# Kernel tuning notes

Hardware: AMD Instinct MI355X
Metric: run time of the kernel (lower is better)

The kernel has to match this reference:

```python
import jax, jax.numpy as jnp
import numpy as np
import math

# Dims: d_model=192, expand=2 -> d_inner=d_ssm=384, headdim=64 -> nheads=6,
# d_state=128, K=4 scan directions, ngroups=1 (directions fused into state dim).
D_MODEL = 192
D_STATE = 128
D_CONV = 3
EXPAND = 2
HEADDIM = 64
CHUNK = 256
D_INNER = EXPAND * D_MODEL          # 384
D_SSM = D_INNER                     # default d_ssm (d_mlp == 0)
NHEADS = D_SSM // HEADDIM           # 6
K = 4                               # scan directions
HTOT = K * NHEADS                   # 24 heads in the fused scan
NSTATE = K * D_STATE                # 512 fused state dim (ngroups=1)
CONV_BC = 2 * D_STATE + NHEADS      # 262
B, H, W = 2, 64, 64


def _dwconv(x, w, b):
    # x: (B,C,H,W), w: (C,1,k,k) depthwise, SAME padding ((k-1)//2)
    y = jax.lax.conv_general_dilated(
        x, w, (1, 1), [(1, 1), (1, 1)],
        feature_group_count=x.shape[1],
        dimension_numbers=('NCHW', 'OIHW', 'NCHW'))
    return y + b[None, :, None, None]


def _ssd(x, dt_raw, A_logs, Bm, Cm, Ds, dt_bias):
    # Mamba2 chunked selective scan (dt_softplus=True, default dt_limit).
    # x: (b,l,h,p)  dt_raw: (b,l,h)  Bm,Cm: (b,l,n) with ngroups=1
    A = -jnp.exp(A_logs)                              # (h,)
    dt = jax.nn.softplus(dt_raw + dt_bias)            # (b,l,h)
    b, l, h, p = x.shape
    n = Bm.shape[-1]
    nc = l // CHUNK
    xc = x.reshape(b, nc, CHUNK, h, p)
    dtc = dt.reshape(b, nc, CHUNK, h)
    Bc = Bm.reshape(b, nc, CHUNK, n)
    Cc = Cm.reshape(b, nc, CHUNK, n)
    dA = dtc * A                                      # (b,nc,cs,h)
    acum = jnp.cumsum(dA, axis=2)
    # intra-chunk (causal, attention-like)
    a_t = jnp.transpose(acum, (0, 1, 3, 2))           # (b,nc,h,cs)
    diff = a_t[..., :, None] - a_t[..., None, :]      # (b,nc,h,i,j)
    causal = jnp.tril(jnp.ones((CHUNK, CHUNK), bool))
    Lmat = jnp.where(causal, jnp.exp(diff), 0.0)
    CB = jnp.einsum('bcin,bcjn->bcij', Cc, Bc)        # (b,nc,i,j)
    M = CB[:, :, None] * Lmat * jnp.transpose(dtc, (0, 1, 3, 2))[:, :, :, None, :]
    y = jnp.einsum('bchij,bcjhp->bcihp', M, xc)
    # chunk-final states
    decay_end = jnp.exp(acum[:, :, -1:, :] - acum)    # (b,nc,cs,h)
    states = jnp.einsum('bcjh,bcjn,bcjhp->bchpn', decay_end * dtc, Bc, xc)
    chunk_decay = jnp.exp(acum[:, :, -1, :])          # (b,nc,h)

    def step(S, inp):
        st, dec = inp
        return S * dec[:, :, None, None] + st, S

    S0 = jnp.zeros((b, h, p, n), x.dtype)
    _, prev = jax.lax.scan(step, S0, (jnp.moveaxis(states, 1, 0),
                                      jnp.moveaxis(chunk_decay, 1, 0)))
    prev = jnp.moveaxis(prev, 0, 1)                   # (b,nc,h,p,n)
    y = y + jnp.einsum('bcih,bcin,bchpn->bcihp', jnp.exp(acum), Cc, prev)
    y = y + xc * Ds[:, None]                          # D skip connection
    return y.reshape(b, l, h, p)


def _branch(u, u_cross, W_skip, W_xs, W_bcdt, conv_xs_w, conv_xs_b,
            conv_bc_w, conv_bc_b, dt_bias, A_logs, Ds, norm_w, W_out):
    Bb, Hh, Ww, _ = u.shape
    L = Hh * Ww
    z = (u @ W_skip).reshape(Bb, L, D_SSM)            # gate (d_mlp == 0)
    xs = jnp.transpose(u @ W_xs, (0, 3, 1, 2))        # (B,d_ssm,H,W)
    xs = jax.nn.silu(_dwconv(xs, conv_xs_w, conv_xs_b))
    bc = jnp.transpose(u_cross @ W_bcdt, (0, 3, 1, 2))
    bc = jax.nn.silu(_dwconv(bc, conv_bc_w, conv_bc_b))
    xbc = jnp.concatenate([xs, bc], axis=1)           # (B,646,H,W)
    C = xbc.shape[1]
    v = xbc.reshape(Bb, C, L)                         # HW raster
    vt = jnp.transpose(xbc, (0, 1, 3, 2)).reshape(Bb, C, L)  # WH raster
    hw = jnp.stack([v, vt], axis=1)                   # (B,2,C,L)
    xbcdt = jnp.concatenate([hw, jnp.flip(hw, axis=-1)], axis=1)  # (B,4,C,L)
    xp = xbcdt[:, :, :D_SSM]
    Bp = xbcdt[:, :, D_SSM:D_SSM + D_STATE]
    Cp = xbcdt[:, :, D_SSM + D_STATE:D_SSM + 2 * D_STATE]
    dtp = xbcdt[:, :, D_SSM + 2 * D_STATE:]
    x = xp.reshape(Bb, K * D_SSM, L).transpose(0, 2, 1).reshape(Bb, L, HTOT, HEADDIM)
    Bm = Bp.reshape(Bb, NSTATE, L).transpose(0, 2, 1)
    Cm = Cp.reshape(Bb, NSTATE, L).transpose(0, 2, 1)
    dt = dtp.reshape(Bb, HTOT, L).transpose(0, 2, 1)
    y = _ssd(x, dt, A_logs, Bm, Cm, Ds, dt_bias)      # (B,L,24,64)
    y = y.reshape(Bb, L, K, D_SSM)
    out_y = y[:, :, 0]
    inv_y = jnp.flip(y[:, :, 2:4], axis=1)            # (B,L,2,d_ssm)
    wh_y = y[:, :, 1].reshape(Bb, Ww, Hh, D_SSM).transpose(0, 2, 1, 3).reshape(Bb, L, D_SSM)
    invwh_y = inv_y[:, :, 1].reshape(Bb, Ww, Hh, D_SSM).transpose(0, 2, 1, 3).reshape(Bb, L, D_SSM)
    yf = out_y + inv_y[:, :, 0] + wh_y + invwh_y
    # gated RMSNorm (norm_before_gate=False, group_size == d_ssm)
    g = yf * jax.nn.silu(z)
    g = g * jax.lax.rsqrt(jnp.mean(g * g, axis=-1, keepdims=True) + 1e-5) * norm_w
    return (g @ W_out).reshape(Bb, Hh, Ww, D_MODEL)


def setup_inputs():
    key = jax.random.key(0)
    ks = jax.random.split(key, 16)
    f = lambda i, s: jax.random.normal(ks[i], s, jnp.float32)
    sc = 0.02
    dt = jnp.exp(jax.random.uniform(ks[10], (NHEADS,)) *
                 (math.log(0.1) - math.log(0.001)) + math.log(0.001))
    dt = jnp.maximum(dt, 1e-4)
    inv_dt = dt + jnp.log(-jnp.expm1(-dt))
    A = jax.random.uniform(ks[11], (NHEADS,), minval=1.0, maxval=16.0)
    return {
        'u1': f(0, (B, H, W, D_MODEL)),
        'u2': f(1, (B, H, W, D_MODEL)),
        'u2_cat_u1': f(2, (B, H, W, D_MODEL)),
        'u1_cat_u2': f(3, (B, H, W, D_MODEL)),
        'W_skip': f(4, (D_MODEL, D_SSM)) * sc,
        'W_xs': f(5, (D_MODEL, D_SSM)) * sc,
        'W_bcdt': f(6, (D_MODEL, CONV_BC)) * sc,
        'conv_xs_w': f(7, (D_SSM, 1, D_CONV, D_CONV)) * sc,
        'conv_xs_b': jnp.zeros((D_SSM,), jnp.float32),
        'conv_bc_w': f(8, (CONV_BC, 1, D_CONV, D_CONV)) * sc,
        'conv_bc_b': jnp.zeros((CONV_BC,), jnp.float32),
        'dt_bias': jnp.tile(inv_dt, K),
        'A_logs': jnp.tile(jnp.log(A), K),
        'Ds': jnp.ones((HTOT,), jnp.float32),
        'norm_w': jnp.ones((D_SSM,), jnp.float32),
        'W_out': f(9, (D_SSM, D_MODEL)) * sc,
    }


def reference(u1, u2, u2_cat_u1, u1_cat_u2, W_skip, W_xs, W_bcdt,
              conv_xs_w, conv_xs_b, conv_bc_w, conv_bc_b,
              dt_bias, A_logs, Ds, norm_w, W_out):
    args = (W_skip, W_xs, W_bcdt, conv_xs_w, conv_xs_b, conv_bc_w,
            conv_bc_b, dt_bias, A_logs, Ds, norm_w, W_out)
    out1 = _branch(u1, u2_cat_u1, *args)
    out2 = _branch(u2, u1_cat_u2, *args)
    return out1, out2
```

## Files before the change

### kernel.cpp

```cpp
#include <hip/hip_runtime.h>
#include <hip/hip_bf16.h>

#define DEV __device__ __forceinline__

static constexpr int LL   = 4096;
static constexpr int GG   = 4;
static constexpr int CBC  = 262;

typedef float f32x4  __attribute__((ext_vector_type(4)));
typedef short bf16x8 __attribute__((ext_vector_type(8)));
typedef short bf16x4v __attribute__((ext_vector_type(4)));
typedef short bf16x2 __attribute__((ext_vector_type(2)));

DEV int map_l(int s, int k) {
    int m = (k & 2) ? (4095 - s) : s;
    if (k & 1) m = ((m & 63) << 6) | (m >> 6);
    return m;
}
DEV float silu_f(float x) { return x / (1.f + __expf(-x)); }
DEV short f2bf(float f) {
    union { __hip_bfloat16 h; short s; } u;
    u.h = __float2bfloat16(f);
    return u.s;
}
DEV float bf2f(short s) {
    return __uint_as_float(((unsigned)(unsigned short)s) << 16);
}
DEV bf16x8 pack8(float4 a, float4 b) {
    bf16x8 r;
    r[0]=f2bf(a.x); r[1]=f2bf(a.y); r[2]=f2bf(a.z); r[3]=f2bf(a.w);
    r[4]=f2bf(b.x); r[5]=f2bf(b.y); r[6]=f2bf(b.z); r[7]=f2bf(b.w);
    return r;
}
DEV bf16x8 load8u(const __hip_bfloat16* p) {
    bf16x4v lo = *(const bf16x4v*)p;
    bf16x4v hi = *(const bf16x4v*)(p + 4);
    bf16x8 r;
    r[0]=lo[0]; r[1]=lo[1]; r[2]=lo[2]; r[3]=lo[3];
    r[4]=hi[0]; r[5]=hi[1]; r[6]=hi[2]; r[7]=hi[3];
    return r;
}
DEV void store16(__hip_bfloat16* p, const float* v) {
    bf16x8 a, b;
    #pragma unroll
    for (int e = 0; e < 8; ++e) { a[e] = f2bf(v[e]); b[e] = f2bf(v[8+e]); }
    *(bf16x8*)p = a;
    *((bf16x8*)p + 1) = b;
}
DEV void storeT(float v, float* p) { *p = v; }
DEV void storeT(float v, __hip_bfloat16* p) { *p = __float2bfloat16(v); }

__global__ void sentinel_k(float* out) { out[0] = 1e30f; }

__global__ void wt_all_k(const float* __restrict__ W_skip, const float* __restrict__ W_xs,
                         const float* __restrict__ W_bcdt, const float* __restrict__ W_out,
                         __hip_bfloat16* __restrict__ Wt)
{
    int idx = blockIdx.x * 256 + threadIdx.x;
    if (idx < 73728) {
        int n = idx / 192, k = idx - n * 192;
        Wt[idx] = __float2bfloat16(W_skip[(size_t)k * 384 + n]);
    } else if (idx < 147456) {
        int r = idx - 73728;
        int n = r / 192, k = r - n * 192;
        Wt[idx] = __float2bfloat16(W_xs[(size_t)k * 384 + n]);
    } else if (idx < 208896) {
        int r = idx - 147456;
        int n = r / 192, k = r - n * 192;
        Wt[idx] = __float2bfloat16(n < 262 ? W_bcdt[(size_t)k * 262 + n] : 0.f);
    } else if (idx < 282624) {
        int r = idx - 208896;
        int n = r / 384, k = r - n * 384;
        Wt[idx] = __float2bfloat16(W_out[(size_t)k * 192 + n]);
    }
}

template<int MODE, typename AT, typename OutT>
__global__ __launch_bounds__(256) void mgemm_k(
    const AT* __restrict__ A0, const AT* __restrict__ A1,
    const __hip_bfloat16* __restrict__ Wt, OutT* __restrict__ C,
    OutT* __restrict__ C2, int N, int Kd)
{
    int i0 = blockIdx.y * 128;
    int j0 = blockIdx.x * 64;
    int t = threadIdx.x;
    int w = t >> 6, lane = t & 63;
    int lr = lane & 15, kq = lane >> 4;
    const AT* arow[2];
    #pragma unroll
    for (int a = 0; a < 2; ++a) {
        int grow = i0 + w * 32 + a * 16 + lr;
        const AT* Ap = (grow < 8192) ? A0 : A1;
        arow[a] = Ap + (size_t)(grow & 8191) * Kd;
    }
    f32x4 acc[2][4] = {};
    for (int k0 = 0; k0 < Kd; k0 += 32) {
        int kb = k0 + kq * 8;
        bf16x8 af[2];
        #pragma unroll
        for (int a = 0; a < 2; ++a) {
            if constexpr (sizeof(AT) == 4)
                af[a] = pack8(*(const float4*)(arow[a] + kb), *(const float4*)(arow[a] + kb + 4));
            else
                af[a] = *(const bf16x8*)(arow[a] + kb);
        }
        #pragma unroll
        for (int b = 0; b < 4; ++b) {
            int n = j0 + b * 16 + lr;
            bf16x8 bfr = *(const bf16x8*)(Wt + (size_t)n * Kd + kb);
            #pragma unroll
            for (int a = 0; a < 2; ++a)
                acc[a][b] = __builtin_amdgcn_mfma_f32_16x16x32_bf16(af[a], bfr, acc[a][b], 0, 0, 0);
        }
    }
    #pragma unroll
    for (int a = 0; a < 2; ++a)
        #pragma unroll
        for (int b = 0; b < 4; ++b)
            #pragma unroll
            for (int r = 0; r < 4; ++r) {
                int row = i0 + w * 32 + a * 16 + kq * 4 + r;
                int col = j0 + b * 16 + lr;
                float v = acc[a][b][r];
                if constexpr (MODE == 0) {
                    if (col < N) storeT(v, &C[(size_t)row * N + col]);
                } else if constexpr (MODE == 1) {
                    if (col < N) storeT(silu_f(v), &C[(size_t)row * N + col]);
                } else {
                    if (col < 384) storeT(silu_f(v), &C[(size_t)row * 384 + col]);
                    else           storeT(v, &C2[(size_t)row * 384 + col - 384]);
                }
            }
}

__global__ __launch_bounds__(256) void xtc_k(const __hip_bfloat16* __restrict__ pre_xs,
                                             const float* __restrict__ cxw,
                                             const float* __restrict__ cxb,
                                             __hip_bfloat16* __restrict__ XtG)
{
    __shared__ float raw[18][18][17];
    __shared__ float ls[16][17][17];
    __shared__ float wsm[16][9];
    __shared__ float bsm[16];
    int bid = blockIdx.x;
    int pct = bid % 24;
    int rest = bid / 24;
    int wt = rest & 3, ht2 = (rest >> 2) & 3, g = rest >> 4;
    int h0 = ht2 * 16, w0 = wt * 16, pc0 = pct * 16;
    int t = threadIdx.x;
    if (t < 144) wsm[t / 9][t % 9] = cxw[(pc0 + t / 9) * 9 + t % 9];
    if (t < 16)  bsm[t] = cxb[pc0 + t];
    for (int i = t; i < 18 * 18 * 16; i += 256) {
        int ch = i & 15;
        int hw = i >> 4;
        int ww2 = hw % 18, hh = hw / 18;
        int gh = h0 - 1 + hh, gw = w0 - 1 + ww2;
        float v = 0.f;
        if ((unsigned)gh < 64u && (unsigned)gw < 64u)
            v = __bfloat162float(pre_xs[((size_t)g * LL + gh * 64 + gw) * 384 + pc0 + ch]);
        raw[hh][ww2][ch] = v;
    }
    __syncthreads();
    {
        int h = t >> 4, w2 = t & 15;
        #pragma unroll 4
        for (int ch = 0; ch < 16; ++ch) {
            float acc = bsm[ch];
            #pragma unroll
            for (int dy = 0; dy < 3; ++dy)
                #pragma unroll
                for (int dx = 0; dx < 3; ++dx)
                    acc += raw[h + dy][w2 + dx][ch] * wsm[ch][dy * 3 + dx];
            ls[h][w2][ch] = silu_f(acc);
        }
    }
    __syncthreads();
    int pc = t >> 4, q = t & 15;
    float v[16];
    size_t rowbase;
    #pragma unroll
    for (int e = 0; e < 16; ++e) v[e] = ls[q][e][pc];
    rowbase = ((size_t)(g * 2 + 0) * 384 + pc0 + pc) * 4096;
    store16(XtG + rowbase + (h0 + q) * 64 + w0, v);
    #pragma unroll
    for (int e = 0; e < 16; ++e) v[e] = ls[e][q][pc];
    rowbase = ((size_t)(g * 2 + 1) * 384 + pc0 + pc) * 4096;
    store16(XtG + rowbase + (w0 + q) * 64 + h0, v);
}

DEV void conv16(const __hip_bfloat16* __restrict__ pre, const float* __restrict__ cw,
                const float* __restrict__ cbia, int g, int h0, int w0, int chb,
                float* smem, float (*wsm)[9], float* bsm, int t)
{
    if (t < 144) wsm[t / 9][t % 9] = cw[(chb + t / 9) * 9 + t % 9];
    if (t < 16)  bsm[t] = cbia[chb + t];
    for (int i = t; i < 18 * 18 * 8; i += 256) {
        int cp = i & 7;
        int hw = i >> 3;
        int ww2 = hw % 18, hh = hw / 18;
        int gh = h0 - 1 + hh, gw = w0 - 1 + ww2;
        float v0 = 0.f, v1 = 0.f;
        if ((unsigned)gh < 64u && (unsigned)gw < 64u) {
            bf16x2 pv = *(const bf16x2*)(pre + ((size_t)g * LL + gh * 64 + gw) * 262 + chb + cp * 2);
            v0 = bf2f(pv[0]); v1 = bf2f(pv[1]);
        }
        smem[(hh * 18 + ww2) * 17 + cp * 2]     = v0;
        smem[(hh * 18 + ww2) * 17 + cp * 2 + 1] = v1;
    }
    __syncthreads();
    int h = t >> 4, w2 = t & 15;
    float out[16];
    #pragma unroll
    for (int ch = 0; ch < 16; ++ch) {
        float acc = bsm[ch];
        #pragma unroll
        for (int dy = 0; dy < 3; ++dy)
            #pragma unroll
            for (int dx = 0; dx < 3; ++dx)
                acc += smem[((h + dy) * 18 + (w2 + dx)) * 17 + ch] * wsm[ch][dy * 3 + dx];
        out[ch] = silu_f(acc);
    }
    __syncthreads();
    #pragma unroll
    for (int ch = 0; ch < 16; ++ch)
        smem[(h * 17 + w2) * 17 + ch] = out[ch];
    __syncthreads();
}

__global__ __launch_bounds__(256) void prep_k(
    const __hip_bfloat16* __restrict__ pre_bc, const float* __restrict__ cbw,
    const float* __restrict__ cbb, const float* __restrict__ dt_bias,
    const float* __restrict__ A_logs, __hip_bfloat16* __restrict__ Bt,
    __hip_bfloat16* __restrict__ Cs, __hip_bfloat16* __restrict__ Bs,
    float* __restrict__ dt_arr, float* __restrict__ ac_arr,
    float* __restrict__ cdecay)
{
    __shared__ float smem[18 * 18 * 17];
    __shared__ float wsm[16][9];
    __shared__ float bsm[16];
    __shared__ float wsum[4];
    int bid = blockIdx.x;
    int t = threadIdx.x;
    if (bid < 2048) {
        int nt = bid & 31;
        int rest = bid >> 5;
        int wt = rest & 3, ht2 = (rest >> 2) & 3, g = rest >> 4;
        int h0 = ht2 * 16, w0 = wt * 16;
        int kd = nt >> 3, ch0 = (nt & 7) * 16;
        conv16(pre_bc, cbw, cbb, g, h0, w0, ch0, smem, wsm, bsm, t);
        int pc = t >> 4, q = t & 15;
        int n = nt * 16 + pc;
        __hip_bfloat16* rowp = Bt + ((size_t)g * 512 + n) * 4096;
        float v[16];
        if (kd == 0) {
            #pragma unroll
            for (int e = 0; e < 16; ++e) v[e] = smem[(q * 17 + e) * 17 + pc];
            store16(rowp + (h0 + q) * 64 + w0, v);
        } else if (kd == 1) {
            #pragma unroll
            for (int e = 0; e < 16; ++e) v[e] = smem[(e * 17 + q) * 17 + pc];
            store16(rowp + (w0 + q) * 64 + h0, v);
        } else if (kd == 2) {
            #pragma unroll
            for (int e = 0; e < 16; ++e) v[e] = smem[(q * 17 + 15 - e) * 17 + pc];
            store16(rowp + 4095 - (h0 + q) * 64 - w0 - 15, v);
        } else {
            #pragma unroll
            for (int e = 0; e < 16; ++e) v[e] = smem[((15 - e) * 17 + q) * 17 + pc];
            store16(rowp + 4095 - (w0 + q) * 64 - h0 - 15, v);
        }
    } else if (bid < 4096) {
        int b2 = bid - 2048;
        int ct = b2 & 31;
        int rest = b2 >> 5;
        int wt = rest & 3, ht2 = (rest >> 2) & 3, g = rest >> 4;
        int h0 = ht2 * 16, w0 = wt * 16;
        bool isB = ct >= 16;
        int ctl = ct & 15;
        int kd = ctl >> 3, ch0 = (ctl & 7) * 16;
        int chb = (isB ? 0 : 128) + ch0;
        conv16(pre_bc, cbw, cbb, g, h0, w0, chb, smem, wsm, bsm, t);
        __hip_bfloat16* dst = isB ? Bs : Cs;
        int h = t >> 4, w2 = t & 15;
        int s = (kd == 0) ? (h0 + h) * 64 + (w0 + w2) : (w0 + w2) * 64 + (h0 + h);
        float v[16];
        #pragma unroll
        for (int e = 0; e < 16; ++e) v[e] = smem[(h * 17 + w2) * 17 + e];
        store16(dst + ((size_t)g * 4096 + s) * 256 + kd * 128 + ch0, v);
    } else {
        int b3 = bid - 4096;
        int ht = b3 % 24;
        int gc = b3 / 24;
        int c = gc & 15, g = gc >> 4;
        int k = ht / 6, h = ht % 6;
        int s = c * 256 + t;
        int l = map_l(s, k);
        int ch = 256 + h;
        float acc = cbb[ch];
        int hh0 = l >> 6, ww0 = l & 63;
        #pragma unroll
        for (int dy = 0; dy < 3; ++dy) {
            int gh = hh0 + dy - 1;
            if ((unsigned)gh >= 64u) continue;
            #pragma unroll
            for (int dx = 0; dx < 3; ++dx) {
                int gw = ww0 + dx - 1;
                if ((unsigned)gw >= 64u) continue;
                acc += __bfloat162float(pre_bc[((size_t)g * LL + gh * 64 + gw) * 262 + ch]) *
                       cbw[ch * 9 + dy * 3 + dx];
            }
        }
        float raw = silu_f(acc) + dt_bias[ht];
        float dtv = raw > 20.f ? raw : log1pf(__expf(raw));
        float dA = dtv * (-__expf(A_logs[ht]));
        float v = dA;
        #pragma unroll
        for (int off = 1; off < 64; off <<= 1) {
            float u = __shfl_up(v, off);
            if ((t & 63) >= off) v += u;
        }
        if ((t & 63) == 63) wsum[t >> 6] = v;
        __syncthreads();
        float add = 0.f;
        #pragma unroll
        for (int w2 = 0; w2 < 3; ++w2)
            if (w2 < (t >> 6)) add += wsum[w2];
        float cum = v + add;
        size_t base = ((size_t)g * 24 + ht) * LL + s;
        dt_arr[base] = dtv;
        ac_arr[base] = cum;
        if (t == 255) cdecay[(g * 24 + ht) * 16 + c] = __expf(cum);
    }
}

__global__ __launch_bounds__(256) void cbst_k(
    const __hip_bfloat16* __restrict__ Cs, const __hip_bfloat16* __restrict__ Bs,
    __hip_bfloat16* __restrict__ CBm,
    const __hip_bfloat16* __restrict__ XtG, const __hip_bfloat16* __restrict__ Bt,
    const float* __restrict__ dt_arr, const float* __restrict__ ac_arr,
    __hip_bfloat16* __restrict__ states)
{
    __shared__ float wsh[256];
    __shared__ short xw[64][264];
    int bid = blockIdx.x;
    int t = threadIdx.x;
    int w = t >> 6, lane = t & 63;
    int lr = lane & 15, kq = lane >> 4;
    if (bid < 256) {
        int jq = bid & 3;
        int gc = bid >> 2;
        int c = gc & 15, g = gc >> 4;
        const __hip_bfloat16* cg = Cs + (size_t)g * 4096 * 256;
        const __hip_bfloat16* bsg = Bs + (size_t)g * 4096 * 256;
        f32x4 acc[4][4] = {};
        for (int ks = 0; ks < 16; ++ks) {
            int n0 = ks * 32 + kq * 8;
            int kd = n0 >> 7, nn = n0 & 127;
            int col = ((kd & 1) << 7) + nn;
            bf16x8 bfr[4];
            #pragma unroll
            for (int jt = 0; jt < 4; ++jt) {
                int j = jq * 64 + jt * 16 + lr;
                int s = c * 256 + j;
                int row = (kd < 2) ? s : 4095 - s;
                bfr[jt] = *(const bf16x8*)(bsg + (size_t)row * 256 + col);
            }
            #pragma unroll
            for (int iq = 0; iq < 4; ++iq) {
                int i = (w * 4 + iq) * 16 + lr;
                int s = c * 256 + i;
                int row = (kd < 2) ? s : 4095 - s;
                bf16x8 af = *(const bf16x8*)(cg + (size_t)row * 256 + col);
                #pragma unroll
                for (int jt = 0; jt < 4; ++jt)
                    acc[iq][jt] = __builtin_amdgcn_mfma_f32_16x16x32_bf16(af, bfr[jt], acc[iq][jt], 0, 0, 0);
            }
        }
        __hip_bfloat16* ob = CBm + (size_t)gc * 65536;
        #pragma unroll
        for (int iq = 0; iq < 4; ++iq)
            #pragma unroll
            for (int jt = 0; jt < 4; ++jt)
                #pragma unroll
                for (int r = 0; r < 4; ++r) {
                    int i = (w * 4 + iq) * 16 + kq * 4 + r;
                    int j = jq * 64 + jt * 16 + lr;
                    ob[(size_t)i * 256 + j] = __float2bfloat16(acc[iq][jt][r]);
                }
        return;
    }
    int sb = bid - 256;
    int task = (sb & 7) * 384 + (sb >> 3);
    int ht = task % 24;
    int rest = task / 24;
    int nh = rest & 1;
    int gc = rest >> 1;
    int c = gc & 15, g = gc >> 4;
    int kd = ht / 6;
    bool rev = kd >= 2;
    int c0 = (ht % 6) * 64;
    int n0 = nh * 256;
    const float* dtp = dt_arr + ((size_t)g * 24 + ht) * LL + c * 256;
    const float* acp = ac_arr + ((size_t)g * 24 + ht) * LL + c * 256;
    float ac_last = acp[255];
    wsh[t] = __expf(ac_last - acp[t]) * dtp[t];
    __syncthreads();
    const __hip_bfloat16* xg = XtG + ((size_t)(g * 2 + (kd & 1)) * 384 + c0) * 4096;
    #pragma unroll
    for (int r8 = 0; r8 < 8; ++r8) {
        int id = t + 256 * r8;
        int p = id >> 5;
        int jc = (id & 31) * 8;
        bf16x8 xv;
        if (!rev) {
            xv = *(const bf16x8*)(xg + (size_t)p * 4096 + c * 256 + jc);
        } else {
            bf16x8 tmp = load8u(xg + (size_t)p * 4096 + 4088 - c * 256 - jc);
            #pragma unroll
            for (int e = 0; e < 8; ++e) xv[e] = tmp[7 - e];
        }
        bf16x8 o;
        #pragma unroll
        for (int e = 0; e < 8; ++e) o[e] = f2bf(bf2f(xv[e]) * wsh[jc + e]);
        *(bf16x8*)&xw[p][jc] = o;
    }
    __syncthreads();
    const __hip_bfloat16* btg = Bt + ((size_t)g * 512 + n0) * 4096;
    f32x4 acc[4][4] = {};
    for (int ks = 0; ks < 8; ++ks) {
        int j0 = ks * 32 + kq * 8;
        bf16x8 af[4];
        #pragma unroll
        for (int pt = 0; pt < 4; ++pt)
            af[pt] = *(const bf16x8*)&xw[pt * 16 + lr][j0];
        #pragma unroll
        for (int nt = 0; nt < 4; ++nt) {
            int nl = (w * 4 + nt) * 16 + lr;
            bf16x8 bv = *(const bf16x8*)(btg + (size_t)nl * 4096 + c * 256 + j0);
            #pragma unroll
            for (int pt = 0; pt < 4; ++pt)
                acc[pt][nt] = __builtin_amdgcn_mfma_f32_16x16x32_bf16(af[pt], bv, acc[pt][nt], 0, 0, 0);
        }
    }
    __hip_bfloat16* ob = states + ((size_t)gc * 24 + ht) * 32768 + n0;
    #pragma unroll
    for (int pt = 0; pt < 4; ++pt)
        #pragma unroll
        for (int nt = 0; nt < 4; ++nt)
            #pragma unroll
            for (int r = 0; r < 4; ++r) {
                int p = pt * 16 + kq * 4 + r;
                int nl = (w * 4 + nt) * 16 + lr;
                ob[(size_t)p * 512 + nl] = __float2bfloat16(acc[pt][nt][r]);
            }
}

__global__ void scan_k(__hip_bfloat16* __restrict__ states, const float* __restrict__ cdecay)
{
    int idx = blockIdx.x * 256 + threadIdx.x;
    int g = idx / 98304;
    int r = idx - g * 98304;
    int ht = r >> 12;
    int pn8 = (r & 4095) * 8;
    const float* cd = cdecay + (g * 24 + ht) * 16;
    __hip_bfloat16* base = states + ((size_t)g * 384 + ht) * 32768 + pn8;
    float S[8] = {};
    #pragma unroll
    for (int c2 = 0; c2 < 16; ++c2) {
        bf16x8* p = (bf16x8*)(base + (size_t)c2 * 786432);
        bf16x8 tmp = *p;
        bf16x8 o;
        float dec = cd[c2];
        #pragma unroll
        for (int e = 0; e < 8; ++e) {
            o[e] = f2bf(S[e]);
            S[e] = S[e] * dec + bf2f(tmp[e]);
        }
        *p = o;
    }
}

__global__ __launch_bounds__(256) void yk(
    const __hip_bfloat16* __restrict__ XtG, const __hip_bfloat16* __restrict__ Cs,
    const __hip_bfloat16* __restrict__ CBm, const __hip_bfloat16* __restrict__ prev,
    const float* __restrict__ dt_arr, const float* __restrict__ ac_arr,
    const float* __restrict__ Ds, __hip_bfloat16* __restrict__ y4)
{
    __shared__ float acs[256], dts[256], ejdt[256];
    __shared__ short xl[64][264];
    int task = (blockIdx.x & 7) * 192 + (blockIdx.x >> 3);
    int ht = task % 24;
    int gc = task / 24;
    int c = gc & 15, g = gc >> 4;
    int kd = ht / 6;
    bool rev = kd >= 2;
    int c0 = (ht % 6) * 64;
    int t = threadIdx.x;
    int w = t >> 6, lane = t & 63;
    int lr = lane & 15, kq = lane >> 4;
    size_t abase = ((size_t)g * 24 + ht) * LL + c * 256;
    float ac_own = ac_arr[abase + t];
    float dt_own = dt_arr[abase + t];
    acs[t] = ac_own;
    dts[t] = dt_own;
    float acb0 = __shfl(ac_own, (t & 63) & ~31);
    ejdt[t] = __expf(acb0 - ac_own) * dt_own;
    const __hip_bfloat16* xg = XtG + ((size_t)(g * 2 + (kd & 1)) * 384 + c0) * 4096;
    #pragma unroll
    for (int r8 = 0; r8 < 8; ++r8) {
        int id = t + 256 * r8;
        int p = id >> 5;
        int jc = (id & 31) * 8;
        bf16x8 xv;
        if (!rev) {
            xv = *(const bf16x8*)(xg + (size_t)p * 4096 + c * 256 + jc);
        } else {
            bf16x8 tmp = load8u(xg + (size_t)p * 4096 + 4088 - c * 256 - jc);
            #pragma unroll
            for (int e = 0; e < 8; ++e) xv[e] = tmp[7 - e];
        }
        *(bf16x8*)&xl[p][jc] = xv;
    }
    __syncthreads();
    const __hip_bfloat16* cbb = CBm + (size_t)gc * 65536;
    const __hip_bfloat16* cg = Cs + (size_t)g * 4096 * 256;
    f32x4 acc[4][4] = {};
    const __hip_bfloat16* pv = prev + ((size_t)gc * 24 + ht) * 32768;
    auto ld2 = [&](int ns, bf16x8* afq, bf16x8* pb) {
        int n0 = ns * 32 + kq * 8;
        int kd2 = n0 >> 7, nn = n0 & 127;
        int col = ((kd2 & 1) << 7) + nn;
        #pragma unroll
        for (int q = 0; q < 4; ++q) {
            int i = (w + 4 * q) * 16 + lr;
            int s = c * 256 + i;
            int row = (kd2 < 2) ? s : 4095 - s;
            afq[q] = *(const bf16x8*)(cg + (size_t)row * 256 + col);
        }
        #pragma unroll
        for (int pt = 0; pt < 4; ++pt)
            pb[pt] = *(const bf16x8*)(pv + (size_t)(pt * 16 + lr) * 512 + n0);
    };
    auto fma2 = [&](bf16x8* afq, bf16x8* pb) {
        #pragma unroll
        for (int q = 0; q < 4; ++q)
            #pragma unroll
            for (int pt = 0; pt < 4; ++pt)
                acc[q][pt] = __builtin_amdgcn_mfma_f32_16x16x32_bf16(afq[q], pb[pt], acc[q][pt], 0, 0, 0);
    };
    {
        bf16x8 afA[4], pbA[4], afB[4], pbB[4];
        ld2(0, afA, pbA);
        #pragma unroll
        for (int ns = 0; ns < 16; ns += 2) {
            if (ns + 1 < 16) ld2(ns + 1, afB, pbB);
            fma2(afA, pbA);
            if (ns + 2 < 16) ld2(ns + 2, afA, pbA);
            fma2(afB, pbB);
        }
    }
    #pragma unroll
    for (int q = 0; q < 4; ++q)
        #pragma unroll
        for (int r = 0; r < 4; ++r) {
            float er = __expf(acs[(w + 4 * q) * 16 + kq * 4 + r]);
            #pragma unroll
            for (int pt = 0; pt < 4; ++pt) acc[q][pt][r] *= er;
        }
    float aci_q[4];
    #pragma unroll
    for (int q = 0; q < 4; ++q) aci_q[q] = acs[(w + 4 * q) * 16 + lr];
    for (int ks = 0; ks < 8; ++ks) {
        int j0 = ks * 32 + kq * 8;
        bf16x8 xb[4];
        #pragma unroll
        for (int pt = 0; pt < 4; ++pt)
            xb[pt] = *(const bf16x8*)&xl[pt * 16 + lr][j0];
        float acb = acs[ks * 32];
        float ej[8];
        #pragma unroll
        for (int e = 0; e < 8; ++e) ej[e] = ejdt[j0 + e];
        #pragma unroll
        for (int q = 0; q < 4; ++q) {
            int rt = w + 4 * q;
            if (rt < 2 * ks) continue;
            int i = rt * 16 + lr;
            float r2 = __expf(aci_q[q] - acb);
            bf16x8 cb8 = *(const bf16x8*)(cbb + (size_t)i * 256 + j0);
            bf16x8 af;
            if (rt >= 2 * ks + 2) {
                #pragma unroll
                for (int e = 0; e < 8; ++e)
                    af[e] = f2bf(r2 * ej[e] * bf2f(cb8[e]));
            } else {
                #pragma unroll
                for (int e = 0; e < 8; ++e) {
                    float coef = r2 * ej[e] * bf2f(cb8[e]);
                    af[e] = (j0 + e <= i) ? f2bf(coef) : (short)0;
                }
            }
            #pragma unroll
            for (int pt = 0; pt < 4; ++pt)
                acc[q][pt] = __builtin_amdgcn_mfma_f32_16x16x32_bf16(af, xb[pt], acc[q][pt], 0, 0, 0);
        }
    }
    float Dsv = Ds[ht];
    __hip_bfloat16* yb = y4 + (((size_t)(g * 4 + kd) * 4096 + c * 256) * 384) + c0;
    #pragma unroll
    for (int q = 0; q < 4; ++q) {
        int rt = w + 4 * q;
        #pragma unroll
        for (int pt = 0; pt < 4; ++pt) {
            int p = pt * 16 + lr;
            int ibase = rt * 16 + kq * 4;
            bf16x4v x4 = *(const bf16x4v*)&xl[p][ibase];
            #pragma unroll
            for (int r = 0; r < 4; ++r) {
                int i = ibase + r;
                float xv = bf2f(x4[r]);
                yb[(size_t)i * 384 + p] = __float2bfloat16(acc[q][pt][r] + Dsv * xv);
            }
        }
    }
}

__global__ __launch_bounds__(128) void gate_k(
    const __hip_bfloat16* __restrict__ y4, const __hip_bfloat16* __restrict__ z_silu,
    const float* __restrict__ norm_w, __hip_bfloat16* __restrict__ gn)
{
    int g = blockIdx.x >> 12;
    int l = blockIdx.x & 4095;
    int t = threadIdx.x;
    int Tl = ((l & 63) << 6) | (l >> 6);
    const __hip_bfloat16* p0 = y4 + ((size_t)(g * 4 + 0) * 4096 + l) * 384;
    const __hip_bfloat16* p1 = y4 + ((size_t)(g * 4 + 1) * 4096 + Tl) * 384;
    const __hip_bfloat16* p2 = y4 + ((size_t)(g * 4 + 2) * 4096 + 4095 - l) * 384;
    const __hip_bfloat16* p3 = y4 + ((size_t)(g * 4 + 3) * 4096 + 4095 - Tl) * 384;
    const __hip_bfloat16* zp = z_silu + ((size_t)g * LL + l) * 384;
    float gc[3]; float ssq = 0.f;
    #pragma unroll
    for (int q = 0; q < 3; ++q) {
        int cdim = t + 128 * q;
        float yf = __bfloat162float(p0[cdim]) + __bfloat162float(p1[cdim]) +
                   __bfloat162float(p2[cdim]) + __bfloat162float(p3[cdim]);
        float v = yf * __bfloat162float(zp[cdim]);
        gc[q] = v;
        ssq += v * v;
    }
    float v = ssq;
    #pragma unroll
    for (int off = 32; off > 0; off >>= 1) v += __shfl_down(v, off);
    __shared__ float tot[2];
    if ((t & 63) == 0) tot[t >> 6] = v;
    __syncthreads();
    float rs = rsqrtf((tot[0] + tot[1]) * (1.f / 384.f) + 1e-5f);
    __hip_bfloat16* gp = gn + ((size_t)g * LL + l) * 384;
    #pragma unroll
    for (int q = 0; q < 3; ++q) {
        int cdim = t + 128 * q;
        gp[cdim] = __float2bfloat16(gc[q] * rs * norm_w[cdim]);
    }
}

extern "C" void kernel_launch(void* const* d_in, const int* in_sizes, int n_in,
                              void* d_out, int out_size, void* d_ws, size_t ws_size,
                              hipStream_t stream)
{
    const float* u1      = (const float*)d_in[0];
    const float* u2      = (const float*)d_in[1];
    const float* u21     = (const float*)d_in[2];
    const float* u12     = (const float*)d_in[3];
    const float* W_skip  = (const float*)d_in[4];
    const float* W_xs    = (const float*)d_in[5];
    const float* W_bcdt  = (const float*)d_in[6];
    const float* cxw     = (const float*)d_in[7];
    const float* cxb     = (const float*)d_in[8];
    const float* cbw     = (const float*)d_in[9];
    const float* cbb     = (const float*)d_in[10];
    const float* dt_bias = (const float*)d_in[11];
    const float* A_logs  = (const float*)d_in[12];
    const float* Ds      = (const float*)d_in[13];
    const float* norm_w  = (const float*)d_in[14];
    const float* W_out   = (const float*)d_in[15];
    float* out = (float*)d_out;

    char* w = (char*)d_ws;
    size_t o_y4  = 0;
    size_t o_st  = o_y4 + 50331648;
    size_t o_z   = o_st + 100663296;
    size_t o_xtg = o_z  + 12582912;
    size_t o_bt  = o_xtg + 25165824;
    size_t o_cs  = o_bt + 16777216;
    size_t o_cbm = o_cs + 8388608;
    size_t o_dt  = o_cbm + 8388608;
    size_t o_ac  = o_dt + 1572864;
    size_t o_cd  = o_ac + 1572864;
    size_t o_wt  = o_cd + 8192;
    size_t o_bs  = o_wt + 589824;
    size_t total = o_bs + 8388608;
    if (total > ws_size) {
        sentinel_k<<<1, 1, 0, stream>>>(out);
        return;
    }
    __hip_bfloat16* y4     = (__hip_bfloat16*)(w + o_y4);
    __hip_bfloat16* states = (__hip_bfloat16*)(w + o_st);
    __hip_bfloat16* z_silu = (__hip_bfloat16*)(w + o_z);
    __hip_bfloat16* XtG    = (__hip_bfloat16*)(w + o_xtg);
    __hip_bfloat16* Bt     = (__hip_bfloat16*)(w + o_bt);
    __hip_bfloat16* Cs     = (__hip_bfloat16*)(w + o_cs);
    __hip_bfloat16* CBm    = (__hip_bfloat16*)(w + o_cbm);
    float*          dt_arr = (float*)(w + o_dt);
    float*          ac_arr = (float*)(w + o_ac);
    float*          cdecay = (float*)(w + o_cd);
    __hip_bfloat16* Wt     = (__hip_bfloat16*)(w + o_wt);
    __hip_bfloat16* Bs     = (__hip_bfloat16*)(w + o_bs);
    __hip_bfloat16* Wt_skip = Wt;
    __hip_bfloat16* Wt_bcdt = Wt + 147456;
    __hip_bfloat16* Wt_out  = Wt + 208896;
    __hip_bfloat16* pre_bc = (__hip_bfloat16*)(w + o_st);
    __hip_bfloat16* pre_xs = (__hip_bfloat16*)(w + o_st + 8650752);
    __hip_bfloat16* gn     = (__hip_bfloat16*)(w + o_st);

    dim3 blk(256);
    wt_all_k<<<dim3(1104), blk, 0, stream>>>(W_skip, W_xs, W_bcdt, W_out, Wt);
    mgemm_k<2, float, __hip_bfloat16><<<dim3(12, 128), blk, 0, stream>>>(
        u1, u2, Wt_skip, z_silu, pre_xs, 768, 192);
    mgemm_k<0, float, __hip_bfloat16><<<dim3(5, 128), blk, 0, stream>>>(
        u21, u12, Wt_bcdt, pre_bc, nullptr, CBC, 192);
    xtc_k<<<dim3(1536), blk, 0, stream>>>(pre_xs, cxw, cxb, XtG);
    prep_k<<<dim3(5632), blk, 0, stream>>>(pre_bc, cbw, cbb, dt_bias, A_logs,
                                           Bt, Cs, Bs, dt_arr, ac_arr, cdecay);
    cbst_k<<<dim3(3328), blk, 0, stream>>>(Cs, Bs, CBm, XtG, Bt, dt_arr, ac_arr, states);
    scan_k<<<dim3(1536), blk, 0, stream>>>(states, cdecay);
    yk<<<dim3(1536), blk, 0, stream>>>(XtG, Cs, CBm, states, dt_arr, ac_arr, Ds, y4);
    gate_k<<<dim3(16384), dim3(128), 0, stream>>>(y4, z_silu, norm_w, gn);
    mgemm_k<0, __hip_bfloat16, float><<<dim3(3, 128), blk, 0, stream>>>(
        gn, gn + (size_t)8192 * 384, Wt_out, out, nullptr, 192, 384);
}
```

Before: 422.8 us.

## Merge input GEMMs and xs-conv into shared launches; fold norm weight into W_out

The two input projection GEMMs become one kernel launch, with the block index picking which GEMM each block runs. The xs depthwise conv+SiLU+transpose kernel is folded into prep_k as an extra block range and reuses a templated conv16 helper. The RMSNorm weight is multiplied into the transposed W_out during weight conversion instead of being applied in gate_k. Together these cut two kernel launches and their tail effects, and drop per-element work in gate_k, at the cost of a larger, more heterogeneous prep_k and a slight change in where bf16 rounding happens.

```diff
diff --git a/kernel.cpp b/kernel.cpp
--- a/kernel.cpp
+++ b/kernel.cpp
@@ -54,7 +54,7 @@
 
 __global__ void wt_all_k(const float* __restrict__ W_skip, const float* __restrict__ W_xs,
                          const float* __restrict__ W_bcdt, const float* __restrict__ W_out,
-                         __hip_bfloat16* __restrict__ Wt)
+                         const float* __restrict__ norm_w, __hip_bfloat16* __restrict__ Wt)
 {
     int idx = blockIdx.x * 256 + threadIdx.x;
     if (idx < 73728) {
@@ -71,18 +71,15 @@
     } else if (idx < 282624) {
         int r = idx - 208896;
         int n = r / 384, k = r - n * 384;
-        Wt[idx] = __float2bfloat16(W_out[(size_t)k * 192 + n]);
+        Wt[idx] = __float2bfloat16(W_out[(size_t)k * 192 + n] * norm_w[k]);
     }
 }
 
 template<int MODE, typename AT, typename OutT>
-__global__ __launch_bounds__(256) void mgemm_k(
-    const AT* __restrict__ A0, const AT* __restrict__ A1,
-    const __hip_bfloat16* __restrict__ Wt, OutT* __restrict__ C,
-    OutT* __restrict__ C2, int N, int Kd)
-{
-    int i0 = blockIdx.y * 128;
-    int j0 = blockIdx.x * 64;
+DEV void mgemm_body(const AT* __restrict__ A0, const AT* __restrict__ A1,
+                    const __hip_bfloat16* __restrict__ Wt, OutT* __restrict__ C,
+                    OutT* __restrict__ C2, int N, int Kd, int i0, int j0)
+{
     int t = threadIdx.x;
     int w = t >> 6, lane = t & 63;
     int lr = lane & 15, kq = lane >> 4;
@@ -133,61 +130,35 @@
             }
 }
 
-__global__ __launch_bounds__(256) void xtc_k(const __hip_bfloat16* __restrict__ pre_xs,
-                                             const float* __restrict__ cxw,
-                                             const float* __restrict__ cxb,
-                                             __hip_bfloat16* __restrict__ XtG)
-{
-    __shared__ float raw[18][18][17];
-    __shared__ float ls[16][17][17];
-    __shared__ float wsm[16][9];
-    __shared__ float bsm[16];
+template<int MODE, typename AT, typename OutT>
+__global__ __launch_bounds__(256) void mgemm_k(
+    const AT* __restrict__ A0, const AT* __restrict__ A1,
+    const __hip_bfloat16* __restrict__ Wt, OutT* __restrict__ C,
+    OutT* __restrict__ C2, int N, int Kd)
+{
+    mgemm_body<MODE, AT, OutT>(A0, A1, Wt, C, C2, N, Kd,
+                               blockIdx.y * 128, blockIdx.x * 64);
+}
+
+__global__ __launch_bounds__(256) void mgemm_in_k(
+    const float* __restrict__ u1, const float* __restrict__ u2,
+    const float* __restrict__ u21, const float* __restrict__ u12,
+    const __hip_bfloat16* __restrict__ Wt_skip, const __hip_bfloat16* __restrict__ Wt_bcdt,
+    __hip_bfloat16* __restrict__ z_silu, __hip_bfloat16* __restrict__ pre_xs,
+    __hip_bfloat16* __restrict__ pre_bc)
+{
     int bid = blockIdx.x;
-    int pct = bid % 24;
-    int rest = bid / 24;
-    int wt = rest & 3, ht2 = (rest >> 2) & 3, g = rest >> 4;
-    int h0 = ht2 * 16, w0 = wt * 16, pc0 = pct * 16;
-    int t = threadIdx.x;
-    if (t < 144) wsm[t / 9][t % 9] = cxw[(pc0 + t / 9) * 9 + t % 9];
-    if (t < 16)  bsm[t] = cxb[pc0 + t];
-    for (int i = t; i < 18 * 18 * 16; i += 256) {
-        int ch = i & 15;
-        int hw = i >> 4;
-        int ww2 = hw % 18, hh = hw / 18;
-        int gh = h0 - 1 + hh, gw = w0 - 1 + ww2;
-        float v = 0.f;
-        if ((unsigned)gh < 64u && (unsigned)gw < 64u)
-            v = __bfloat162float(pre_xs[((size_t)g * LL + gh * 64 + gw) * 384 + pc0 + ch]);
-        raw[hh][ww2][ch] = v;
-    }
-    __syncthreads();
-    {
-        int h = t >> 4, w2 = t & 15;
-        #pragma unroll 4
-        for (int ch = 0; ch < 16; ++ch) {
-            float acc = bsm[ch];
-            #pragma unroll
-            for (int dy = 0; dy < 3; ++dy)
-                #pragma unroll
-                for (int dx = 0; dx < 3; ++dx)
-                    acc += raw[h + dy][w2 + dx][ch] * wsm[ch][dy * 3 + dx];
-            ls[h][w2][ch] = silu_f(acc);
-        }
-    }
-    __syncthreads();
-    int pc = t >> 4, q = t & 15;
-    float v[16];
-    size_t rowbase;
-    #pragma unroll
-    for (int e = 0; e < 16; ++e) v[e] = ls[q][e][pc];
-    rowbase = ((size_t)(g * 2 + 0) * 384 + pc0 + pc) * 4096;
-    store16(XtG + rowbase + (h0 + q) * 64 + w0, v);
-    #pragma unroll
-    for (int e = 0; e < 16; ++e) v[e] = ls[e][q][pc];
-    rowbase = ((size_t)(g * 2 + 1) * 384 + pc0 + pc) * 4096;
-    store16(XtG + rowbase + (w0 + q) * 64 + h0, v);
-}
-
+    if (bid < 1536) {
+        mgemm_body<2, float, __hip_bfloat16>(u1, u2, Wt_skip, z_silu, pre_xs,
+                                             768, 192, (bid / 12) * 128, (bid % 12) * 64);
+    } else {
+        int b = bid - 1536;
+        mgemm_body<0, float, __hip_bfloat16>(u21, u12, Wt_bcdt, pre_bc, nullptr,
+                                             CBC, 192, (b / 5) * 128, (b % 5) * 64);
+    }
+}
+
+template<int STRIDE>
 DEV void conv16(const __hip_bfloat16* __restrict__ pre, const float* __restrict__ cw,
                 const float* __restrict__ cbia, int g, int h0, int w0, int chb,
                 float* smem, float (*wsm)[9], float* bsm, int t)
@@ -201,7 +172,7 @@
         int gh = h0 - 1 + hh, gw = w0 - 1 + ww2;
         float v0 = 0.f, v1 = 0.f;
         if ((unsigned)gh < 64u && (unsigned)gw < 64u) {
-            bf16x2 pv = *(const bf16x2*)(pre + ((size_t)g * LL + gh * 64 + gw) * 262 + chb + cp * 2);
+            bf16x2 pv = *(const bf16x2*)(pre + ((size_t)g * LL + gh * 64 + gw) * STRIDE + chb + cp * 2);
             v0 = bf2f(pv[0]); v1 = bf2f(pv[1]);
         }
         smem[(hh * 18 + ww2) * 17 + cp * 2]     = v0;
@@ -229,9 +200,11 @@
 
 __global__ __launch_bounds__(256) void prep_k(
     const __hip_bfloat16* __restrict__ pre_bc, const float* __restrict__ cbw,
-    const float* __restrict__ cbb, const float* __restrict__ dt_bias,
-    const float* __restrict__ A_logs, __hip_bfloat16* __restrict__ Bt,
-    __hip_bfloat16* __restrict__ Cs, __hip_bfloat16* __restrict__ Bs,
+    const float* __restrict__ cbb, const __hip_bfloat16* __restrict__ pre_xs,
+    const float* __restrict__ cxw, const float* __restrict__ cxb,
+    const float* __restrict__ dt_bias, const float* __restrict__ A_logs,
+    __hip_bfloat16* __restrict__ Bt, __hip_bfloat16* __restrict__ Cs,
+    __hip_bfloat16* __restrict__ Bs, __hip_bfloat16* __restrict__ XtG,
     float* __restrict__ dt_arr, float* __restrict__ ac_arr,
     float* __restrict__ cdecay)
 {
@@ -247,7 +220,7 @@
         int wt = rest & 3, ht2 = (rest >> 2) & 3, g = rest >> 4;
         int h0 = ht2 * 16, w0 = wt * 16;
         int kd = nt >> 3, ch0 = (nt & 7) * 16;
-        conv16(pre_bc, cbw, cbb, g, h0, w0, ch0, smem, wsm, bsm, t);
+        conv16<262>(pre_bc, cbw, cbb, g, h0, w0, ch0, smem, wsm, bsm, t);
         int pc = t >> 4, q = t & 15;
         int n = nt * 16 + pc;
         __hip_bfloat16* rowp = Bt + ((size_t)g * 512 + n) * 4096;
@@ -279,7 +252,7 @@
         int ctl = ct & 15;
         int kd = ctl >> 3, ch0 = (ctl & 7) * 16;
         int chb = (isB ? 0 : 128) + ch0;
-        conv16(pre_bc, cbw, cbb, g, h0, w0, chb, smem, wsm, bsm, t);
+        conv16<262>(pre_bc, cbw, cbb, g, h0, w0, chb, smem, wsm, bsm, t);
         __hip_bfloat16* dst = isB ? Bs : Cs;
         int h = t >> 4, w2 = t & 15;
         int s = (kd == 0) ? (h0 + h) * 64 + (w0 + w2) : (w0 + w2) * 64 + (h0 + h);
@@ -287,7 +260,7 @@
         #pragma unroll
         for (int e = 0; e < 16; ++e) v[e] = smem[(h * 17 + w2) * 17 + e];
         store16(dst + ((size_t)g * 4096 + s) * 256 + kd * 128 + ch0, v);
-    } else {
+    } else if (bid < 5632) {
         int b3 = bid - 4096;
         int ht = b3 % 24;
         int gc = b3 / 24;
@@ -330,6 +303,24 @@
         dt_arr[base] = dtv;
         ac_arr[base] = cum;
         if (t == 255) cdecay[(g * 24 + ht) * 16 + c] = __expf(cum);
+    } else {
+        int b4 = bid - 5632;
+        int pct = b4 % 24;
+        int rest = b4 / 24;
+        int wt = rest & 3, ht2 = (rest >> 2) & 3, g = rest >> 4;
+        int h0 = ht2 * 16, w0 = wt * 16, pc0 = pct * 16;
+        conv16<384>(pre_xs, cxw, cxb, g, h0, w0, pc0, smem, wsm, bsm, t);
+        int pc = t >> 4, q = t & 15;
+        float v[16];
+        size_t rowbase;
+        #pragma unroll
+        for (int e = 0; e < 16; ++e) v[e] = smem[(q * 17 + e) * 17 + pc];
+        rowbase = ((size_t)(g * 2 + 0) * 384 + pc0 + pc) * 4096;
+        store16(XtG + rowbase + (h0 + q) * 64 + w0, v);
+        #pragma unroll
+        for (int e = 0; e < 16; ++e) v[e] = smem[(e * 17 + q) * 17 + pc];
+        rowbase = ((size_t)(g * 2 + 1) * 384 + pc0 + pc) * 4096;
+        store16(XtG + rowbase + (w0 + q) * 64 + h0, v);
     }
 }
 
@@ -626,7 +617,7 @@
 
 __global__ __launch_bounds__(128) void gate_k(
     const __hip_bfloat16* __restrict__ y4, const __hip_bfloat16* __restrict__ z_silu,
-    const float* __restrict__ norm_w, __hip_bfloat16* __restrict__ gn)
+    __hip_bfloat16* __restrict__ gn)
 {
     int g = blockIdx.x >> 12;
     int l = blockIdx.x & 4095;
@@ -658,7 +649,7 @@
     #pragma unroll
     for (int q = 0; q < 3; ++q) {
         int cdim = t + 128 * q;
-        gp[cdim] = __float2bfloat16(gc[q] * rs * norm_w[cdim]);
+        gp[cdim] = __float2bfloat16(gc[q] * rs);
     }
 }
 
@@ -722,18 +713,16 @@
     __hip_bfloat16* gn     = (__hip_bfloat16*)(w + o_st);
 
     dim3 blk(256);
-    wt_all_k<<<dim3(1104), blk, 0, stream>>>(W_skip, W_xs, W_bcdt, W_out, Wt);
-    mgemm_k<2, float, __hip_bfloat16><<<dim3(12, 128), blk, 0, stream>>>(
-        u1, u2, Wt_skip, z_silu, pre_xs, 768, 192);
-    mgemm_k<0, float, __hip_bfloat16><<<dim3(5, 128), blk, 0, stream>>>(
-        u21, u12, Wt_bcdt, pre_bc, nullptr, CBC, 192);
-    xtc_k<<<dim3(1536), blk, 0, stream>>>(pre_xs, cxw, cxb, XtG);
-    prep_k<<<dim3(5632), blk, 0, stream>>>(pre_bc, cbw, cbb, dt_bias, A_logs,
-                                           Bt, Cs, Bs, dt_arr, ac_arr, cdecay);
+    wt_all_k<<<dim3(1104), blk, 0, stream>>>(W_skip, W_xs, W_bcdt, W_out, norm_w, Wt);
+    mgemm_in_k<<<dim3(2176), blk, 0, stream>>>(u1, u2, u21, u12, Wt_skip, Wt_bcdt,
+                                               z_silu, pre_xs, pre_bc);
+    prep_k<<<dim3(7168), blk, 0, stream>>>(pre_bc, cbw, cbb, pre_xs, cxw, cxb,
+                                           dt_bias, A_logs, Bt, Cs, Bs, XtG,
+                                           dt_arr, ac_arr, cdecay);
     cbst_k<<<dim3(3328), blk, 0, stream>>>(Cs, Bs, CBm, XtG, Bt, dt_arr, ac_arr, states);
     scan_k<<<dim3(1536), blk, 0, stream>>>(states, cdecay);
     yk<<<dim3(1536), blk, 0, stream>>>(XtG, Cs, CBm, states, dt_arr, ac_arr, Ds, y4);
-    gate_k<<<dim3(16384), dim3(128), 0, stream>>>(y4, z_silu, norm_w, gn);
+    gate_k<<<dim3(16384), dim3(128), 0, stream>>>(y4, z_silu, gn);
     mgemm_k<0, __hip_bfloat16, float><<<dim3(3, 128), blk, 0, stream>>>(
         gn, gn + (size_t)8192 * 384, Wt_out, out, nullptr, 192, 384);
 }
```

New measurement: 403.4 us. 4.6% less time.
